# Kernel tuning notes

Measured on AMD Instinct MI355X. Metric: run time of the kernel, lower is better.

## Reference

```python
import jax, jax.numpy as jnp
import numpy as np

EPS = 1e-12
W_MAX = 0.8
ALPHA_MAX = 1.5
T = 10
ETA = 0.2
ALPHA_SCALE = 1.0
N = 50000
IN_DIM = 512
HID = 256
C = 8
EH = 64
E2 = 400000  # undirected pairs; E = 2*E2 directed edges


def setup_inputs() -> dict:
    key = jax.random.key(0)
    ks = jax.random.split(key, 12)
    x = jax.random.normal(ks[0], (N, IN_DIM), jnp.float32)
    src0 = jax.random.randint(ks[1], (E2,), 0, N)
    dst0 = jax.random.randint(ks[2], (E2,), 0, N)
    edge_index = jnp.concatenate([jnp.stack([src0, dst0]), jnp.stack([dst0, src0])], axis=1)
    rev = jnp.concatenate([jnp.arange(E2) + E2, jnp.arange(E2)])
    def lin(k, i, o):
        return jax.random.normal(k, (i, o), jnp.float32) * (2.0 / i) ** 0.5
    enc_w1 = lin(ks[3], IN_DIM, HID); enc_b1 = jnp.zeros((HID,), jnp.float32)
    enc_w2 = lin(ks[4], HID, C); enc_b2 = jnp.zeros((C,), jnp.float32)
    edge_w1 = lin(ks[5], 2 * HID + 2, EH); edge_b1 = jnp.zeros((EH,), jnp.float32)
    edge_w2 = lin(ks[6], EH, 1); edge_b2 = jnp.zeros((1,), jnp.float32)
    bound = (6.0 / (C + C)) ** 0.5  # xavier_uniform
    R_raw = jax.random.uniform(ks[7], (C, C), jnp.float32, -bound, bound) + 0.5 * jnp.eye(C, dtype=jnp.float32)
    R_scale_log = jnp.float32(0.0)
    msg_logit = jnp.float32(-3.0)
    return dict(x=x, edge_index=edge_index, rev=rev,
                enc_w1=enc_w1, enc_b1=enc_b1, enc_w2=enc_w2, enc_b2=enc_b2,
                edge_w1=edge_w1, edge_b1=edge_b1, edge_w2=edge_w2, edge_b2=edge_b2,
                R_raw=R_raw, R_scale_log=R_scale_log, msg_logit=msg_logit)


def reference(x, edge_index, rev, enc_w1, enc_b1, enc_w2, enc_b2,
              edge_w1, edge_b1, edge_w2, edge_b2, R_raw, R_scale_log, msg_logit):
    num_nodes = x.shape[0]
    src, dst = edge_index[0], edge_index[1]
    # unary encoder (mlp type, eval mode -> no dropout)
    h = jax.nn.relu(x @ enc_w1 + enc_b1)
    logits = h @ enc_w2 + enc_b2
    log_phi = jax.nn.log_softmax(logits, axis=-1)  # [N, C]
    # structural edge features from out-degree of src
    deg = jax.ops.segment_sum(jnp.ones_like(src, jnp.float32), src, num_segments=num_nodes)
    logdeg = jnp.log(deg + 1.0)
    a, b = logdeg[src], logdeg[dst]
    struct = jnp.stack([a + b, jnp.abs(a - b)], axis=-1)  # [E, 2]
    # learned symmetric edge weights -> per-edge kernel K
    hs, hd = h[src], h[dst]
    edge_in = jnp.concatenate([hs * hd, jnp.abs(hs - hd), struct], axis=-1)  # [E, 2H+2]
    eh = jax.nn.relu(edge_in @ edge_w1 + edge_b1)
    w_raw = (eh @ edge_w2 + edge_b2)[:, 0]
    w = W_MAX * jax.nn.sigmoid(w_raw)
    w = 0.5 * (w + w[rev])
    R = 0.5 * (R_raw + R_raw.T)
    R = (jax.nn.softplus(R_scale_log) + 1e-06) * jnp.tanh(R)
    K = jnp.exp(w[:, None, None] * R[None])  # [E, C, C]
    degc = jnp.maximum(deg, 1.0)
    edge_norm = (degc[src] * degc[dst]) ** -0.5  # [E]
    alpha = ALPHA_MAX * jax.nn.sigmoid(msg_logit) * ALPHA_SCALE
    lp_src = log_phi[src]
    m = jax.nn.softmax(lp_src, axis=-1)  # init_unary=True

    def step(m, _):
        f = jnp.einsum('ec,ecd->ed', m, K)
        log_f = jnp.log(jnp.maximum(f, EPS)) * edge_norm[:, None]
        sum_in = jax.ops.segment_sum(log_f, dst, num_segments=num_nodes)
        excl = sum_in[src] - log_f[rev]
        m_new = jax.nn.softmax(lp_src + alpha * excl, axis=-1)
        m = (1.0 - ETA) * m + ETA * m_new
        m = jnp.maximum(m, EPS)
        m = m / m.sum(axis=-1, keepdims=True)
        return m, None

    m, _ = jax.lax.scan(step, m, None, length=T)
    # beliefs
    f = jnp.einsum('ec,ecd->ed', m, K)
    log_f = jnp.log(jnp.maximum(f, EPS)) * edge_norm[:, None]
    sum_in = jax.ops.segment_sum(log_f, dst, num_segments=num_nodes)
    beliefs = jax.nn.softmax(log_phi + alpha * sum_in, axis=-1)
    return beliefs
```

## Files before the change

### kernel.cpp

```cpp
#include <hip/hip_runtime.h>
#include <cstddef>
#include <cstdint>

typedef _Float16 h4 __attribute__((ext_vector_type(4)));
typedef _Float16 h8 __attribute__((ext_vector_type(8)));
typedef float    f4 __attribute__((ext_vector_type(4)));
typedef int      i4 __attribute__((ext_vector_type(4)));

#define NN      50000
#define IND     512
#define HIDN    256
#define E2P     400000
#define EDD     800000
#define NBLK    196
#define EBLK    1563

#define OFF_HF16    ((size_t)0)
#define OFF_LOGF    ((size_t)0)
#define OFF_Z       ((size_t)25600000)
#define OFF_DEG     ((size_t)28800000)
#define OFF_LOGDEG  ((size_t)29000000)
#define OFF_DEGC    ((size_t)29200000)
#define OFF_BASE    ((size_t)29400000)
#define OFF_CNT     ((size_t)29600000)
#define OFF_BLK     ((size_t)29800000)
#define OFF_WT      ((size_t)29804096)
#define OFF_BT      ((size_t)30066240)
#define OFF_RS      ((size_t)30135872)
#define OFF_WSYM    ((size_t)30136384)
#define OFF_POS     ((size_t)31736384)
#define OFF_ORDER   ((size_t)34936384)
#define OFF_BASE2   ((size_t)36536384)
#define OFF_OFS2    ((size_t)36736384)
#define OFF_PRC     ((size_t)36936384)
#define OFF_WN      ((size_t)43336384)
#define OFF_M       ((size_t)46536384)
#define WS_NEED     ((size_t)59336384)

__global__ void k_deg(const int* __restrict__ ei, int* __restrict__ deg) {
    int e = blockIdx.x * 256 + threadIdx.x;
    atomicAdd(&deg[ei[e]], 1);
}

__global__ void k_node(const int* __restrict__ deg, float* __restrict__ logdeg,
                       float* __restrict__ degc) {
    int n = blockIdx.x * 256 + threadIdx.x;
    if (n < NN) {
        float d = (float)deg[n];
        logdeg[n] = logf(d + 1.0f);
        degc[n]   = fmaxf(d, 1.0f);
    }
}

__global__ void k_scan1(const int* __restrict__ deg, int* __restrict__ incl,
                        int* __restrict__ blk) {
    __shared__ int sm[256];
    int i = blockIdx.x * 256 + threadIdx.x;
    int v = (i < NN) ? deg[i] : 0;
    sm[threadIdx.x] = v;
    __syncthreads();
    for (int off = 1; off < 256; off <<= 1) {
        int t = (threadIdx.x >= off) ? sm[threadIdx.x - off] : 0;
        __syncthreads();
        sm[threadIdx.x] += t;
        __syncthreads();
    }
    if (i < NN) incl[i] = sm[threadIdx.x];
    if (threadIdx.x == 255) blk[blockIdx.x] = sm[255];
}

__global__ void k_scan2(int* __restrict__ blk) {
    __shared__ int sm[256];
    int v = (threadIdx.x < NBLK) ? blk[threadIdx.x] : 0;
    sm[threadIdx.x] = v;
    __syncthreads();
    for (int off = 1; off < 256; off <<= 1) {
        int t = (threadIdx.x >= off) ? sm[threadIdx.x - off] : 0;
        __syncthreads();
        sm[threadIdx.x] += t;
        __syncthreads();
    }
    if (threadIdx.x < NBLK) blk[threadIdx.x] = sm[threadIdx.x];
}

__global__ void k_scan3(const int* __restrict__ incl, const int* __restrict__ deg,
                        const int* __restrict__ blk, int* __restrict__ base) {
    int i = blockIdx.x * 256 + threadIdx.x;
    if (i < NN) {
        int off = (blockIdx.x > 0) ? blk[blockIdx.x - 1] : 0;
        base[i] = off + incl[i] - deg[i];
    }
}

__global__ void k_pos(const int* __restrict__ ei, const int* __restrict__ base,
                      int* __restrict__ cnt, int* __restrict__ pos) {
    int e = blockIdx.x * 256 + threadIdx.x;
    int dstn = ei[EDD + e];
    pos[e] = base[dstn] + atomicAdd(&cnt[dstn], 1);
}

__global__ void k_cnt2(const int* __restrict__ ei, int* __restrict__ cnt2) {
    int p = blockIdx.x * 256 + threadIdx.x;
    if (p < E2P) atomicAdd(&cnt2[ei[p]], 1);
}

__global__ void k_order(const int* __restrict__ ei, const int* __restrict__ base2,
                        int* __restrict__ ofs2, int* __restrict__ order) {
    int p = blockIdx.x * 256 + threadIdx.x;
    if (p < E2P) {
        int s = ei[p];
        order[base2[s] + atomicAdd(&ofs2[s], 1)] = p;
    }
}

__global__ void k_prep(const float* __restrict__ enc_w1, const float* __restrict__ edge_w1,
                       const float* __restrict__ R_raw, const float* __restrict__ Rsl,
                       const float* __restrict__ mlog,
                       _Float16* __restrict__ Wt, _Float16* __restrict__ Bt,
                       float* __restrict__ Rs) {
    int gid = blockIdx.x * 256 + threadIdx.x;
    if (gid < 256 * 512) {
        int n = gid >> 9, k = gid & 511;
        Wt[n * 512 + k] = (_Float16)enc_w1[k * 256 + n];
        return;
    }
    int g2 = gid - 256 * 512;
    if (g2 < 64 * 544) {
        int n = g2 / 544, k = g2 - n * 544;
        float v = 0.0f;
        if (k < 512) {
            int tm = k >> 5, r = k & 31;
            int qq = r >> 3, jj = (r >> 1) & 3, typ = k & 1;
            int c = (tm >> 1) * 32 + qq * 8 + (tm & 1) * 4 + jj;
            v = edge_w1[(typ ? 256 + c : c) * 64 + n];
        } else if (k < 514) {
            v = edge_w1[k * 64 + n];
        }
        Bt[n * 544 + k] = (_Float16)v;
        return;
    }
    int g3 = g2 - 64 * 544;
    if (g3 < 64) {
        int c = g3 >> 3, d = g3 & 7;
        float rv = 0.5f * (R_raw[c * 8 + d] + R_raw[d * 8 + c]);
        float s  = log1pf(expf(Rsl[0])) + 1e-6f;
        Rs[g3] = s * tanhf(rv);
        return;
    }
    if (g3 == 64) {
        Rs[64] = 1.5f / (1.0f + expf(-mlog[0]));
    }
}

__global__ __launch_bounds__(256) void k_enc(const float* __restrict__ x,
                                             const _Float16* __restrict__ Wt,
                                             const float* __restrict__ b1,
                                             _Float16* __restrict__ hf) {
    __shared__ _Float16 XL[64 * 40];
    __shared__ _Float16 WL[256 * 40];
    const int tid = threadIdx.x;
    const int wid = tid >> 6;
    const int lane = tid & 63;
    const int l15 = lane & 15;
    const int q = lane >> 4;
    const int m0 = blockIdx.x * 64;

    f4 acc[16];
#pragma unroll
    for (int i = 0; i < 16; i++) acc[i] = (f4){0.f, 0.f, 0.f, 0.f};

    const int xr = tid >> 2;
    const int xs = tid & 3;
    const int gr = m0 + xr;

    for (int kt = 0; kt < 16; kt++) {
        __syncthreads();
        f4 xv0 = (f4){0, 0, 0, 0}, xv1 = (f4){0, 0, 0, 0};
        if (gr < NN) {
            const f4* xp = (const f4*)(x + (size_t)gr * IND + kt * 32 + xs * 8);
            xv0 = xp[0]; xv1 = xp[1];
        }
        h8 xh;
#pragma unroll
        for (int u = 0; u < 4; u++) { xh[u] = (_Float16)xv0[u]; xh[4 + u] = (_Float16)xv1[u]; }
        *(h8*)&XL[xr * 40 + xs * 8] = xh;
#pragma unroll
        for (int rep = 0; rep < 4; rep++) {
            int cid = rep * 256 + tid;
            int n = cid >> 2;
            int off = (cid & 3) * 8;
            h8 wv = *(const h8*)(Wt + (size_t)n * IND + kt * 32 + off);
            *(h8*)&WL[n * 40 + off] = wv;
        }
        __syncthreads();
        h8 a = *(const h8*)&XL[(wid * 16 + l15) * 40 + q * 8];
#pragma unroll
        for (int nt = 0; nt < 16; nt++) {
            h8 b = *(const h8*)&WL[(nt * 16 + l15) * 40 + q * 8];
            acc[nt] = __builtin_amdgcn_mfma_f32_16x16x32_f16(a, b, acc[nt], 0, 0, 0);
        }
    }
#pragma unroll
    for (int nt = 0; nt < 16; nt++) {
        int col = nt * 16 + l15;
        float bv = b1[col];
#pragma unroll
        for (int reg = 0; reg < 4; reg++) {
            int row = m0 + wid * 16 + q * 4 + reg;
            if (row < NN) {
                float v = acc[nt][reg] + bv;
                hf[(size_t)row * HIDN + col] = (_Float16)fmaxf(v, 0.f);
            }
        }
    }
}

__global__ void k_logits(const _Float16* __restrict__ hf, const float* __restrict__ w2,
                         const float* __restrict__ b2, float* __restrict__ Z) {
    __shared__ float w2L[2048];
    for (int i = threadIdx.x; i < 2048; i += 256) w2L[i] = w2[i];
    __syncthreads();
    int n = blockIdx.x * 256 + threadIdx.x;
    if (n >= NN) return;
    float sum[8];
#pragma unroll
    for (int c = 0; c < 8; c++) sum[c] = b2[c];
    for (int kb = 0; kb < 32; kb++) {
        h8 hv = *(const h8*)(hf + (size_t)n * HIDN + kb * 8);
#pragma unroll
        for (int u = 0; u < 8; u++) {
            float hx = (float)hv[u];
            const float* wr = &w2L[(kb * 8 + u) * 8];
#pragma unroll
            for (int c = 0; c < 8; c++) sum[c] += hx * wr[c];
        }
    }
    float mx = sum[0];
#pragma unroll
    for (int c = 1; c < 8; c++) mx = fmaxf(mx, sum[c]);
    float se = 0.f;
#pragma unroll
    for (int c = 0; c < 8; c++) se += __expf(sum[c] - mx);
    float lse = __logf(se);
#pragma unroll
    for (int c = 0; c < 8; c++) Z[(size_t)n * 16 + c] = sum[c] - mx - lse;
}

__global__ __launch_bounds__(256) void k_edge(const int* __restrict__ ei,
        const _Float16* __restrict__ hf, const float* __restrict__ logdeg,
        const _Float16* __restrict__ BtG, const float* __restrict__ eb1,
        const float* __restrict__ ew2, const float* __restrict__ eb2,
        float* __restrict__ wsym) {
    __shared__ _Float16 BtL[64 * 136];
    const int tid = threadIdx.x;
    const int wid = tid >> 6;
    const int lane = tid & 63;
    const int l15 = lane & 15;
    const int q = lane >> 4;
    const int eb = blockIdx.x * 128;

    int sidx[2], didx[2];
    float la[2], lb[2];
#pragma unroll
    for (int mt = 0; mt < 2; mt++) {
        int e = eb + wid * 32 + mt * 16 + l15;
        sidx[mt] = ei[e];
        didx[mt] = ei[EDD + e];
        la[mt] = logdeg[sidx[mt]];
        lb[mt] = logdeg[didx[mt]];
    }

    f4 acc[2][4];
#pragma unroll
    for (int a = 0; a < 2; a++)
#pragma unroll
        for (int b = 0; b < 4; b++) acc[a][b] = (f4){0.f, 0.f, 0.f, 0.f};

    const _Float16* hq = hf + q * 8;
    h8 curS[2], curD[2];
#pragma unroll
    for (int mt = 0; mt < 2; mt++) {
        curS[mt] = *(const h8*)(hq + (size_t)sidx[mt] * HIDN);
        curD[mt] = *(const h8*)(hq + (size_t)didx[mt] * HIDN);
    }

    for (int ph = 0; ph < 4; ph++) {
        __syncthreads();
        {
            const int r = tid & 63;
            const int cb = tid >> 6;
            const int kbase = ph * 128;
#pragma unroll
            for (int i = 0; i < 4; i++) {
                int ck = cb + i * 4;
                *(h8*)&BtL[r * 136 + ck * 8] =
                    *(const h8*)(BtG + (size_t)r * 544 + kbase + ck * 8);
            }
        }
        __syncthreads();
#pragma unroll
        for (int kk2 = 0; kk2 < 2; kk2++) {
            const int kk = ph * 2 + kk2;
            h8 nxtS[2], nxtD[2];
            if (kk < 7) {
                const int c1 = (kk + 1) * 32;
#pragma unroll
                for (int mt = 0; mt < 2; mt++) {
                    nxtS[mt] = *(const h8*)(hq + (size_t)sidx[mt] * HIDN + c1);
                    nxtD[mt] = *(const h8*)(hq + (size_t)didx[mt] * HIDN + c1);
                }
            }
            const int ko = kk2 * 64 + q * 8;
            {
                h8 a0[2];
#pragma unroll
                for (int mt = 0; mt < 2; mt++) {
#pragma unroll
                    for (int j = 0; j < 4; j++) {
                        float x1 = (float)curS[mt][j], x2 = (float)curD[mt][j];
                        a0[mt][2 * j]     = (_Float16)(x1 * x2);
                        a0[mt][2 * j + 1] = (_Float16)fabsf(x1 - x2);
                    }
                }
                h8 bf[4];
#pragma unroll
                for (int nt = 0; nt < 4; nt++)
                    bf[nt] = *(const h8*)&BtL[(nt * 16 + l15) * 136 + ko];
#pragma unroll
                for (int mt = 0; mt < 2; mt++)
#pragma unroll
                    for (int nt = 0; nt < 4; nt++)
                        acc[mt][nt] = __builtin_amdgcn_mfma_f32_16x16x32_f16(a0[mt], bf[nt], acc[mt][nt], 0, 0, 0);
            }
            {
                h8 a1[2];
#pragma unroll
                for (int mt = 0; mt < 2; mt++) {
#pragma unroll
                    for (int j = 0; j < 4; j++) {
                        float x1 = (float)curS[mt][4 + j], x2 = (float)curD[mt][4 + j];
                        a1[mt][2 * j]     = (_Float16)(x1 * x2);
                        a1[mt][2 * j + 1] = (_Float16)fabsf(x1 - x2);
                    }
                }
                h8 bf[4];
#pragma unroll
                for (int nt = 0; nt < 4; nt++)
                    bf[nt] = *(const h8*)&BtL[(nt * 16 + l15) * 136 + ko + 32];
#pragma unroll
                for (int mt = 0; mt < 2; mt++)
#pragma unroll
                    for (int nt = 0; nt < 4; nt++)
                        acc[mt][nt] = __builtin_amdgcn_mfma_f32_16x16x32_f16(a1[mt], bf[nt], acc[mt][nt], 0, 0, 0);
            }
            if (kk < 7) {
#pragma unroll
                for (int mt = 0; mt < 2; mt++) { curS[mt] = nxtS[mt]; curD[mt] = nxtD[mt]; }
            }
        }
    }

    __syncthreads();
    {
        const int r = tid & 63, ck = tid >> 6;
        *(h8*)&BtL[r * 136 + ck * 8] = *(const h8*)(BtG + (size_t)r * 544 + 512 + ck * 8);
    }
    __syncthreads();
    {
        h8 bf[4];
#pragma unroll
        for (int nt = 0; nt < 4; nt++)
            bf[nt] = *(const h8*)&BtL[(nt * 16 + l15) * 136 + q * 8];
#pragma unroll
        for (int mt = 0; mt < 2; mt++) {
            h8 a = (h8){0, 0, 0, 0, 0, 0, 0, 0};
            if (q == 0) {
                a[0] = (_Float16)(la[mt] + lb[mt]);
                a[1] = (_Float16)fabsf(la[mt] - lb[mt]);
            }
#pragma unroll
            for (int nt = 0; nt < 4; nt++)
                acc[mt][nt] = __builtin_amdgcn_mfma_f32_16x16x32_f16(a, bf[nt], acc[mt][nt], 0, 0, 0);
        }
    }

    float b1v[4], w2v[4];
#pragma unroll
    for (int nt = 0; nt < 4; nt++) {
        int col = nt * 16 + l15;
        b1v[nt] = eb1[col];
        w2v[nt] = ew2[col];
    }
    const float b2s = eb2[0];
    float part[2][4];
#pragma unroll
    for (int mt = 0; mt < 2; mt++)
#pragma unroll
        for (int reg = 0; reg < 4; reg++) {
            float s = 0.f;
#pragma unroll
            for (int nt = 0; nt < 4; nt++) {
                float v = acc[mt][nt][reg] + b1v[nt];
                s += fmaxf(v, 0.f) * w2v[nt];
            }
            part[mt][reg] = s;
        }
#pragma unroll
    for (int off = 1; off < 16; off <<= 1)
#pragma unroll
        for (int mt = 0; mt < 2; mt++)
#pragma unroll
            for (int reg = 0; reg < 4; reg++)
                part[mt][reg] += __shfl_xor(part[mt][reg], off, 64);
    if (l15 == 0) {
#pragma unroll
        for (int mt = 0; mt < 2; mt++)
#pragma unroll
            for (int reg = 0; reg < 4; reg++) {
                int er = eb + wid * 32 + mt * 16 + q * 4 + reg;
                if (er < E2P) {
                    float xr = part[mt][reg] + b2s;
                    wsym[er] = 0.8f / (1.0f + __expf(-xr));
                }
            }
    }
}


__device__ __forceinline__ void kprod(const float* __restrict__ RsL, float w,
                                      const float* me, const float* mr,
                                      float* fe, float* fr) {
#pragma unroll
    for (int d = 0; d < 8; d++) { fe[d] = 0.f; fr[d] = 0.f; }
#pragma unroll
    for (int c = 0; c < 8; c++) {
        {
            float kv = __expf(w * RsL[c * 8 + c]);
            fe[c] += me[c] * kv;
            fr[c] += mr[c] * kv;
        }
#pragma unroll
        for (int d = c + 1; d < 8; d++) {
            float kv = __expf(w * RsL[c * 8 + d]);
            fe[d] += me[c] * kv; fr[d] += mr[c] * kv;
            fe[c] += me[d] * kv; fr[c] += mr[d] * kv;
        }
    }
}

__global__ __launch_bounds__(256) void k_init(const int* __restrict__ ei,
        const float* __restrict__ wsymb, const float* __restrict__ degc,
        const float* __restrict__ Rs, const float* __restrict__ Z,
        const int* __restrict__ pos, const int* __restrict__ order,
        i4* __restrict__ prc, float2* __restrict__ wn,
        _Float16* __restrict__ M, _Float16* __restrict__ logf) {
    __shared__ float RsL[64];
    const int tid = threadIdx.x;
    if (tid < 64) RsL[tid] = Rs[tid];
    __syncthreads();
    int i = blockIdx.x * 256 + tid;
    if (i >= E2P) return;
    int p = order[i];
    int sp = ei[p], dp = ei[EDD + p];
    float w = wsymb[p];
    float nrm = rsqrtf(degc[sp] * degc[dp]);
    int pz0 = pos[p], pz1 = pos[E2P + p];
    prc[i] = (i4){sp, dp, pz0, pz1};
    wn[i] = make_float2(w, nrm);
    const f4* Zs = (const f4*)(Z + (size_t)sp * 16);
    const f4* Zd = (const f4*)(Z + (size_t)dp * 16);
    f4 ls0 = Zs[0], ls1 = Zs[1], ld0 = Zd[0], ld1 = Zd[1];
    float lps[8], lpd[8];
#pragma unroll
    for (int u = 0; u < 4; u++) { lps[u] = ls0[u]; lps[4+u] = ls1[u]; lpd[u] = ld0[u]; lpd[4+u] = ld1[u]; }
    float me[8], mr[8];
    {
        float mx = lps[0], mx2 = lpd[0];
#pragma unroll
        for (int d = 1; d < 8; d++) { mx = fmaxf(mx, lps[d]); mx2 = fmaxf(mx2, lpd[d]); }
        float s = 0.f, s2 = 0.f;
#pragma unroll
        for (int d = 0; d < 8; d++) { me[d] = __expf(lps[d] - mx); s += me[d];
                                      mr[d] = __expf(lpd[d] - mx2); s2 += mr[d]; }
        float rs = 1.f / s, rs2 = 1.f / s2;
#pragma unroll
        for (int d = 0; d < 8; d++) { me[d] *= rs; mr[d] *= rs2; }
    }
    {
        h8 mh, mh2;
#pragma unroll
        for (int d = 0; d < 8; d++) { mh[d] = (_Float16)me[d]; mh2[d] = (_Float16)mr[d]; }
        *(h8*)(M + (size_t)i * 16)     = mh;
        *(h8*)(M + (size_t)i * 16 + 8) = mh2;
    }
    float fe[8], fr[8];
    kprod(RsL, w, me, mr, fe, fr);
    h8 le, lr;
#pragma unroll
    for (int d = 0; d < 8; d++) {
        le[d] = (_Float16)(__logf(fmaxf(fe[d], 1e-12f)) * nrm);
        lr[d] = (_Float16)(__logf(fmaxf(fr[d], 1e-12f)) * nrm);
    }
    *(h8*)(logf + (size_t)pz0 * 8) = le;
    *(h8*)(logf + (size_t)pz1 * 8) = lr;
}

__global__ __launch_bounds__(256) void k_bpF(const i4* __restrict__ prc,
        const float2* __restrict__ wn, const float* __restrict__ Rs,
        const float* __restrict__ Z, _Float16* __restrict__ M,
        _Float16* __restrict__ logf) {
    __shared__ float RsL[64];
    const int tid = threadIdx.x;
    if (tid < 64) RsL[tid] = Rs[tid];
    __syncthreads();
    int i = blockIdx.x * 256 + tid;
    if (i >= E2P) return;
    i4 c4 = prc[i];
    const int sp = c4[0], dp = c4[1], pz0 = c4[2], pz1 = c4[3];
    float2 wnv = wn[i];
    const float w = wnv.x, nrm = wnv.y;
    const float alpha = Rs[64];
    h8 mhe = *(const h8*)(M + (size_t)i * 16);
    h8 mhr = *(const h8*)(M + (size_t)i * 16 + 8);
    float me[8], mr[8];
#pragma unroll
    for (int d = 0; d < 8; d++) { me[d] = (float)mhe[d]; mr[d] = (float)mhr[d]; }
    float fe[8], fr[8];
    kprod(RsL, w, me, mr, fe, fr);
    float lfe[8], lfr[8];
#pragma unroll
    for (int d = 0; d < 8; d++) {
        lfe[d] = __logf(fmaxf(fe[d], 1e-12f)) * nrm;
        lfr[d] = __logf(fmaxf(fr[d], 1e-12f)) * nrm;
    }
    const f4* Zs = (const f4*)(Z + (size_t)sp * 16);
    const f4* Zd = (const f4*)(Z + (size_t)dp * 16);
    f4 ls0 = Zs[0], ls1 = Zs[1], ss0 = Zs[2], ss1 = Zs[3];
    f4 ld0 = Zd[0], ld1 = Zd[1], sd0 = Zd[2], sd1 = Zd[3];
    float te[8], tr[8];
#pragma unroll
    for (int u = 0; u < 4; u++) {
        te[u]     = ls0[u] + alpha * (ss0[u] - lfr[u]);
        te[4 + u] = ls1[u] + alpha * (ss1[u] - lfr[4 + u]);
        tr[u]     = ld0[u] + alpha * (sd0[u] - lfe[u]);
        tr[4 + u] = ld1[u] + alpha * (sd1[u] - lfe[4 + u]);
    }
    float m1[8], m2[8];
    {
        float mx = te[0], mx2 = tr[0];
#pragma unroll
        for (int d = 1; d < 8; d++) { mx = fmaxf(mx, te[d]); mx2 = fmaxf(mx2, tr[d]); }
        float s = 0.f, s2 = 0.f;
#pragma unroll
        for (int d = 0; d < 8; d++) { m1[d] = __expf(te[d] - mx); s += m1[d];
                                      m2[d] = __expf(tr[d] - mx2); s2 += m2[d]; }
        float rs = 1.f / s, rs2 = 1.f / s2;
        float t1 = 0.f, t2 = 0.f;
#pragma unroll
        for (int d = 0; d < 8; d++) {
            m1[d] = fmaxf(0.8f * me[d] + 0.2f * m1[d] * rs, 1e-12f);  t1 += m1[d];
            m2[d] = fmaxf(0.8f * mr[d] + 0.2f * m2[d] * rs2, 1e-12f); t2 += m2[d];
        }
        float rt1 = 1.f / t1, rt2 = 1.f / t2;
#pragma unroll
        for (int d = 0; d < 8; d++) { m1[d] *= rt1; m2[d] *= rt2; }
    }
    {
        h8 mh, mh2;
#pragma unroll
        for (int d = 0; d < 8; d++) { mh[d] = (_Float16)m1[d]; mh2[d] = (_Float16)m2[d]; }
        *(h8*)(M + (size_t)i * 16)     = mh;
        *(h8*)(M + (size_t)i * 16 + 8) = mh2;
    }
    float fe2[8], fr2[8];
    kprod(RsL, w, m1, m2, fe2, fr2);
    h8 le, lr;
#pragma unroll
    for (int d = 0; d < 8; d++) {
        le[d] = (_Float16)(__logf(fmaxf(fe2[d], 1e-12f)) * nrm);
        lr[d] = (_Float16)(__logf(fmaxf(fr2[d], 1e-12f)) * nrm);
    }
    *(h8*)(logf + (size_t)pz0 * 8) = le;
    *(h8*)(logf + (size_t)pz1 * 8) = lr;
}

__global__ void k_sum(const _Float16* __restrict__ logf, const int* __restrict__ base,
                      const int* __restrict__ deg, float* __restrict__ Z,
                      const float* __restrict__ Rs, float* __restrict__ out, int fin) {
    int g = blockIdx.x * 256 + threadIdx.x;
    int n = g >> 3;
    if (n >= NN) return;
    int j = threadIdx.x & 7;
    int b = base[n], cnt = deg[n];
    float acc[8];
#pragma unroll
    for (int d = 0; d < 8; d++) acc[d] = 0.f;
    for (int s = j; s < cnt; s += 8) {
        h8 v = *(const h8*)(logf + (size_t)(b + s) * 8);
#pragma unroll
        for (int d = 0; d < 8; d++) acc[d] += (float)v[d];
    }
    int lane = threadIdx.x & 63;
    float v4[4], v2[2], r;
    {
        bool hi = (lane & 4) != 0;
#pragma unroll
        for (int i = 0; i < 4; i++) {
            float send = hi ? acc[i] : acc[i + 4];
            float recv = __shfl_xor(send, 4, 64);
            v4[i] = (hi ? acc[i + 4] : acc[i]) + recv;
        }
    }
    {
        bool hi = (lane & 2) != 0;
#pragma unroll
        for (int i = 0; i < 2; i++) {
            float send = hi ? v4[i] : v4[i + 2];
            float recv = __shfl_xor(send, 2, 64);
            v2[i] = (hi ? v4[i + 2] : v4[i]) + recv;
        }
    }
    {
        bool hi = (lane & 1) != 0;
        float send = hi ? v2[0] : v2[1];
        float recv = __shfl_xor(send, 1, 64);
        r = (hi ? v2[1] : v2[0]) + recv;
    }
    if (!fin) {
        Z[(size_t)n * 16 + 8 + j] = r;
    } else {
        float alpha = Rs[64];
        float v = Z[(size_t)n * 16 + j] + alpha * r;
        float mx = v;
        mx = fmaxf(mx, __shfl_xor(mx, 1, 64));
        mx = fmaxf(mx, __shfl_xor(mx, 2, 64));
        mx = fmaxf(mx, __shfl_xor(mx, 4, 64));
        float ex = __expf(v - mx);
        float s = ex;
        s += __shfl_xor(s, 1, 64); s += __shfl_xor(s, 2, 64); s += __shfl_xor(s, 4, 64);
        out[(size_t)n * 8 + j] = ex / s;
    }
}

extern "C" void kernel_launch(void* const* d_in, const int* in_sizes, int n_in,
                              void* d_out, int out_size, void* d_ws, size_t ws_size,
                              hipStream_t stream) {
    if (ws_size < WS_NEED) return;
    const float* x        = (const float*)d_in[0];
    const int*   ei       = (const int*)d_in[1];
    const float* enc_w1   = (const float*)d_in[3];
    const float* enc_b1   = (const float*)d_in[4];
    const float* enc_w2   = (const float*)d_in[5];
    const float* enc_b2   = (const float*)d_in[6];
    const float* edge_w1  = (const float*)d_in[7];
    const float* edge_b1  = (const float*)d_in[8];
    const float* edge_w2  = (const float*)d_in[9];
    const float* edge_b2  = (const float*)d_in[10];
    const float* R_raw    = (const float*)d_in[11];
    const float* Rsl      = (const float*)d_in[12];
    const float* mlog     = (const float*)d_in[13];

    char* ws = (char*)d_ws;
    _Float16* hf     = (_Float16*)(ws + OFF_HF16);
    _Float16* logfb  = (_Float16*)(ws + OFF_LOGF);
    float* Zb        = (float*)(ws + OFF_Z);
    int*   deg       = (int*)  (ws + OFF_DEG);
    float* logdeg    = (float*)(ws + OFF_LOGDEG);
    float* degc      = (float*)(ws + OFF_DEGC);
    int*   baseA     = (int*)  (ws + OFF_BASE);
    int*   cnt       = (int*)  (ws + OFF_CNT);
    int*   blk       = (int*)  (ws + OFF_BLK);
    _Float16* Wt     = (_Float16*)(ws + OFF_WT);
    _Float16* Bt     = (_Float16*)(ws + OFF_BT);
    float* Rs        = (float*)(ws + OFF_RS);
    float* wsym      = (float*)(ws + OFF_WSYM);
    int*   pos       = (int*)  (ws + OFF_POS);
    int*   order     = (int*)  (ws + OFF_ORDER);
    int*   base2     = (int*)  (ws + OFF_BASE2);
    int*   ofs2      = (int*)  (ws + OFF_OFS2);
    i4*    prc       = (i4*)   (ws + OFF_PRC);
    float2* wnb      = (float2*)(ws + OFF_WN);
    _Float16* Mb     = (_Float16*)(ws + OFF_M);
    float* outp      = (float*)d_out;

    hipMemsetAsync(deg, 0, (size_t)NN * 4, stream);
    k_deg<<<dim3(EDD / 256), dim3(256), 0, stream>>>(ei, deg);
    k_node<<<dim3(NBLK), dim3(256), 0, stream>>>(deg, logdeg, degc);
    k_prep<<<dim3((256 * 512 + 64 * 544 + 65 + 255) / 256), dim3(256), 0, stream>>>(
        enc_w1, edge_w1, R_raw, Rsl, mlog, Wt, Bt, Rs);
    k_scan1<<<dim3(NBLK), dim3(256), 0, stream>>>(deg, cnt , blk);
    k_scan2<<<dim3(1), dim3(256), 0, stream>>>(blk);
    k_scan3<<<dim3(NBLK), dim3(256), 0, stream>>>(cnt, deg, blk, baseA);
    hipMemsetAsync(cnt, 0, (size_t)NN * 4, stream);
    k_pos<<<dim3(EDD / 256), dim3(256), 0, stream>>>(ei, baseA, cnt, pos);
    hipMemsetAsync(ofs2, 0, (size_t)NN * 4, stream);
    k_cnt2<<<dim3(EBLK), dim3(256), 0, stream>>>(ei, ofs2);
    k_scan1<<<dim3(NBLK), dim3(256), 0, stream>>>(ofs2, cnt, blk);
    k_scan2<<<dim3(1), dim3(256), 0, stream>>>(blk);
    k_scan3<<<dim3(NBLK), dim3(256), 0, stream>>>(cnt, ofs2, blk, base2);
    hipMemsetAsync(ofs2, 0, (size_t)NN * 4, stream);
    k_order<<<dim3(EBLK), dim3(256), 0, stream>>>(ei, base2, ofs2, order);
    k_enc<<<dim3((NN + 63) / 64), dim3(256), 0, stream>>>(x, Wt, enc_b1, hf);
    k_logits<<<dim3(NBLK), dim3(256), 0, stream>>>(hf, enc_w2, enc_b2, Zb);
    k_edge<<<dim3(E2P / 128), dim3(256), 0, stream>>>(ei, hf, logdeg, Bt, edge_b1,
                                                      edge_w2, edge_b2, wsym);
    k_init<<<dim3(EBLK), dim3(256), 0, stream>>>(ei, wsym, degc, Rs, Zb, pos, order,
                                                 prc, wnb, Mb, logfb);
    k_sum<<<dim3((NN * 8 + 255) / 256), dim3(256), 0, stream>>>(logfb, baseA, deg, Zb,
                                                                Rs, outp, 0);
    for (int t = 0; t < 10; t++) {
        k_bpF<<<dim3(EBLK), dim3(256), 0, stream>>>(prc, wnb, Rs, Zb, Mb, logfb);
        k_sum<<<dim3((NN * 8 + 255) / 256), dim3(256), 0, stream>>>(logfb, baseA, deg, Zb,
                                                                    Rs, outp, (t == 9) ? 1 : 0);
    }
    (void)in_sizes; (void)n_in; (void)out_size;
}
```

Baseline: 798.7 us.

## Sort edges by source for edge MLP, reuse stored log_f in BP step

```diff
diff --git a/kernel.cpp b/kernel.cpp
--- a/kernel.cpp
+++ b/kernel.cpp
@@ -35,11 +35,15 @@
 #define OFF_PRC     ((size_t)36936384)
 #define OFF_WN      ((size_t)43336384)
 #define OFF_M       ((size_t)46536384)
-#define WS_NEED     ((size_t)59336384)
-
-__global__ void k_deg(const int* __restrict__ ei, int* __restrict__ deg) {
+#define OFF_EIS     ((size_t)59336384)
+#define WS_NEED     ((size_t)62536384)
+
+__global__ void k_deg(const int* __restrict__ ei, int* __restrict__ deg,
+                      int* __restrict__ cnt2) {
     int e = blockIdx.x * 256 + threadIdx.x;
-    atomicAdd(&deg[ei[e]], 1);
+    int v = ei[e];
+    atomicAdd(&deg[v], 1);
+    if (e < E2P) atomicAdd(&cnt2[v], 1);
 }
 
 __global__ void k_node(const int* __restrict__ deg, float* __restrict__ logdeg,
@@ -99,17 +103,21 @@
     pos[e] = base[dstn] + atomicAdd(&cnt[dstn], 1);
 }
 
-__global__ void k_cnt2(const int* __restrict__ ei, int* __restrict__ cnt2) {
-    int p = blockIdx.x * 256 + threadIdx.x;
-    if (p < E2P) atomicAdd(&cnt2[ei[p]], 1);
-}
-
 __global__ void k_order(const int* __restrict__ ei, const int* __restrict__ base2,
                         int* __restrict__ ofs2, int* __restrict__ order) {
     int p = blockIdx.x * 256 + threadIdx.x;
     if (p < E2P) {
         int s = ei[p];
         order[base2[s] + atomicAdd(&ofs2[s], 1)] = p;
+    }
+}
+
+__global__ void k_gath(const int* __restrict__ ei, const int* __restrict__ order,
+                       int2* __restrict__ eiS) {
+    int i = blockIdx.x * 256 + threadIdx.x;
+    if (i < E2P) {
+        int p = order[i];
+        eiS[i] = make_int2(ei[p], ei[EDD + p]);
     }
 }
 
@@ -246,11 +254,11 @@
     for (int c = 0; c < 8; c++) Z[(size_t)n * 16 + c] = sum[c] - mx - lse;
 }
 
-__global__ __launch_bounds__(256) void k_edge(const int* __restrict__ ei,
+__global__ __launch_bounds__(256) void k_edge(const int2* __restrict__ eiS,
         const _Float16* __restrict__ hf, const float* __restrict__ logdeg,
         const _Float16* __restrict__ BtG, const float* __restrict__ eb1,
         const float* __restrict__ ew2, const float* __restrict__ eb2,
-        float* __restrict__ wsym) {
+        float* __restrict__ wsym2) {
     __shared__ _Float16 BtL[64 * 136];
     const int tid = threadIdx.x;
     const int wid = tid >> 6;
@@ -264,8 +272,9 @@
 #pragma unroll
     for (int mt = 0; mt < 2; mt++) {
         int e = eb + wid * 32 + mt * 16 + l15;
-        sidx[mt] = ei[e];
-        didx[mt] = ei[EDD + e];
+        int2 sd = eiS[e];
+        sidx[mt] = sd.x;
+        didx[mt] = sd.y;
         la[mt] = logdeg[sidx[mt]];
         lb[mt] = logdeg[didx[mt]];
     }
@@ -420,7 +429,7 @@
                 int er = eb + wid * 32 + mt * 16 + q * 4 + reg;
                 if (er < E2P) {
                     float xr = part[mt][reg] + b2s;
-                    wsym[er] = 0.8f / (1.0f + __expf(-xr));
+                    wsym2[er] = 0.8f / (1.0f + __expf(-xr));
                 }
             }
     }
@@ -448,8 +457,8 @@
     }
 }
 
-__global__ __launch_bounds__(256) void k_init(const int* __restrict__ ei,
-        const float* __restrict__ wsymb, const float* __restrict__ degc,
+__global__ __launch_bounds__(256) void k_init(const int2* __restrict__ eiS,
+        const float* __restrict__ wsym2, const float* __restrict__ degc,
         const float* __restrict__ Rs, const float* __restrict__ Z,
         const int* __restrict__ pos, const int* __restrict__ order,
         i4* __restrict__ prc, float2* __restrict__ wn,
@@ -461,8 +470,9 @@
     int i = blockIdx.x * 256 + tid;
     if (i >= E2P) return;
     int p = order[i];
-    int sp = ei[p], dp = ei[EDD + p];
-    float w = wsymb[p];
+    int2 sd = eiS[i];
+    int sp = sd.x, dp = sd.y;
+    float w = wsym2[i];
     float nrm = rsqrtf(degc[sp] * degc[dp]);
     int pz0 = pos[p], pz1 = pos[E2P + p];
     prc[i] = (i4){sp, dp, pz0, pz1};
@@ -520,18 +530,15 @@
     float2 wnv = wn[i];
     const float w = wnv.x, nrm = wnv.y;
     const float alpha = Rs[64];
+    h8 lfh0 = *(const h8*)(logf + (size_t)pz0 * 8);
+    h8 lfh1 = *(const h8*)(logf + (size_t)pz1 * 8);
     h8 mhe = *(const h8*)(M + (size_t)i * 16);
     h8 mhr = *(const h8*)(M + (size_t)i * 16 + 8);
-    float me[8], mr[8];
-#pragma unroll
-    for (int d = 0; d < 8; d++) { me[d] = (float)mhe[d]; mr[d] = (float)mhr[d]; }
-    float fe[8], fr[8];
-    kprod(RsL, w, me, mr, fe, fr);
-    float lfe[8], lfr[8];
+    float me[8], mr[8], lfe[8], lfr[8];
 #pragma unroll
     for (int d = 0; d < 8; d++) {
-        lfe[d] = __logf(fmaxf(fe[d], 1e-12f)) * nrm;
-        lfr[d] = __logf(fmaxf(fr[d], 1e-12f)) * nrm;
+        me[d] = (float)mhe[d];  mr[d] = (float)mhr[d];
+        lfe[d] = (float)lfh0[d]; lfr[d] = (float)lfh1[d];
     }
     const f4* Zs = (const f4*)(Z + (size_t)sp * 16);
     const f4* Zd = (const f4*)(Z + (size_t)dp * 16);
@@ -673,7 +680,7 @@
     _Float16* Wt     = (_Float16*)(ws + OFF_WT);
     _Float16* Bt     = (_Float16*)(ws + OFF_BT);
     float* Rs        = (float*)(ws + OFF_RS);
-    float* wsym      = (float*)(ws + OFF_WSYM);
+    float* wsym2     = (float*)(ws + OFF_WSYM);
     int*   pos       = (int*)  (ws + OFF_POS);
     int*   order     = (int*)  (ws + OFF_ORDER);
     int*   base2     = (int*)  (ws + OFF_BASE2);
@@ -681,10 +688,12 @@
     i4*    prc       = (i4*)   (ws + OFF_PRC);
     float2* wnb      = (float2*)(ws + OFF_WN);
     _Float16* Mb     = (_Float16*)(ws + OFF_M);
+    int2*  eiS       = (int2*) (ws + OFF_EIS);
     float* outp      = (float*)d_out;
 
     hipMemsetAsync(deg, 0, (size_t)NN * 4, stream);
-    k_deg<<<dim3(EDD / 256), dim3(256), 0, stream>>>(ei, deg);
+    hipMemsetAsync(ofs2, 0, (size_t)NN * 4, stream);
+    k_deg<<<dim3(EDD / 256), dim3(256), 0, stream>>>(ei, deg, ofs2);
     k_node<<<dim3(NBLK), dim3(256), 0, stream>>>(deg, logdeg, degc);
     k_prep<<<dim3((256 * 512 + 64 * 544 + 65 + 255) / 256), dim3(256), 0, stream>>>(
         enc_w1, edge_w1, R_raw, Rsl, mlog, Wt, Bt, Rs);
@@ -693,18 +702,17 @@
     k_scan3<<<dim3(NBLK), dim3(256), 0, stream>>>(cnt, deg, blk, baseA);
     hipMemsetAsync(cnt, 0, (size_t)NN * 4, stream);
     k_pos<<<dim3(EDD / 256), dim3(256), 0, stream>>>(ei, baseA, cnt, pos);
-    hipMemsetAsync(ofs2, 0, (size_t)NN * 4, stream);
-    k_cnt2<<<dim3(EBLK), dim3(256), 0, stream>>>(ei, ofs2);
     k_scan1<<<dim3(NBLK), dim3(256), 0, stream>>>(ofs2, cnt, blk);
     k_scan2<<<dim3(1), dim3(256), 0, stream>>>(blk);
     k_scan3<<<dim3(NBLK), dim3(256), 0, stream>>>(cnt, ofs2, blk, base2);
     hipMemsetAsync(ofs2, 0, (size_t)NN * 4, stream);
     k_order<<<dim3(EBLK), dim3(256), 0, stream>>>(ei, base2, ofs2, order);
+    k_gath<<<dim3(EBLK), dim3(256), 0, stream>>>(ei, order, eiS);
     k_enc<<<dim3((NN + 63) / 64), dim3(256), 0, stream>>>(x, Wt, enc_b1, hf);
     k_logits<<<dim3(NBLK), dim3(256), 0, stream>>>(hf, enc_w2, enc_b2, Zb);
-    k_edge<<<dim3(E2P / 128), dim3(256), 0, stream>>>(ei, hf, logdeg, Bt, edge_b1,
-                                                      edge_w2, edge_b2, wsym);
-    k_init<<<dim3(EBLK), dim3(256), 0, stream>>>(ei, wsym, degc, Rs, Zb, pos, order,
+    k_edge<<<dim3(E2P / 128), dim3(256), 0, stream>>>(eiS, hf, logdeg, Bt, edge_b1,
+                                                      edge_w2, edge_b2, wsym2);
+    k_init<<<dim3(EBLK), dim3(256), 0, stream>>>(eiS, wsym2, degc, Rs, Zb, pos, order,
                                                  prc, wnb, Mb, logfb);
     k_sum<<<dim3((NN * 8 + 255) / 256), dim3(256), 0, stream>>>(logfb, baseA, deg, Zb,
                                                                 Rs, outp, 0);
```

Measured after the change: 820.0 us. 1.03x slower.
